# Kernel tuning notes

Measured on AMD Instinct MI355X. Metric: run time of the kernel, lower is better.

## Reference

```python
import jax, jax.numpy as jnp
import numpy as np


def _ln(x, w, b):
    m = x.mean(-1, keepdims=True)
    v = ((x - m) ** 2).mean(-1, keepdims=True)
    return (x - m) / jnp.sqrt(v + 1e-5) * w + b


def setup_inputs() -> dict:
    key = jax.random.key(0)
    ks = jax.random.split(key, 8)
    N, C, H, W = 2, 64, 128, 128
    heads, ksz = 2, 7
    C4 = 4 * C
    p = lambda k, shape: jax.random.normal(k, shape, dtype=jnp.float32) * 0.02
    return {
        "x": jax.random.normal(ks[0], (N, C, H, W), dtype=jnp.float32),
        "qkv_w": p(ks[1], (3 * C, C)),
        "qkv_b": jnp.zeros((3 * C,), jnp.float32),
        "proj_w": p(ks[2], (C, C)),
        "proj_b": jnp.zeros((C,), jnp.float32),
        "rpb": p(ks[3], (heads, 2 * ksz - 1, 2 * ksz - 1)),
        "ln1_w": jnp.ones((C,), jnp.float32),
        "ln1_b": jnp.zeros((C,), jnp.float32),
        "ln2_w": jnp.ones((C,), jnp.float32),
        "ln2_b": jnp.zeros((C,), jnp.float32),
        "fc1_w": p(ks[4], (C4, C)),
        "fc1_b": jnp.zeros((C4,), jnp.float32),
        "fc2_w": p(ks[5], (C, C4)),
        "fc2_b": jnp.zeros((C,), jnp.float32),
    }


def reference(x, qkv_w, qkv_b, proj_w, proj_b, rpb, ln1_w, ln1_b, ln2_w, ln2_b,
              fc1_w, fc1_b, fc2_w, fc2_b):
    N, C, H, W = x.shape
    heads = rpb.shape[0]
    ksz = (rpb.shape[1] + 1) // 2  # kernel size from (2k-1) bias table
    dh = C // heads

    xt = x.transpose(0, 2, 3, 1).reshape(N, H * W, C)  # n (h w) c
    shortcut = xt
    xn = _ln(xt, ln1_w, ln1_b).reshape(N, H, W, C)

    # qkv projection -> (3, N, heads, H, W, dh)
    qkv = (xn @ qkv_w.T + qkv_b).reshape(N, H, W, 3, heads, dh)
    qkv = qkv.transpose(3, 0, 4, 1, 2, 5)
    q = qkv[0] * (dh ** -0.5)
    k = qkv[1]
    v = qkv[2]

    # NATTEN neighborhood: window start clamped so every query sees k x k keys
    sh = jnp.clip(jnp.arange(H) - ksz // 2, 0, H - ksz)
    sw = jnp.clip(jnp.arange(W) - ksz // 2, 0, W - ksz)
    rows = sh[:, None] + jnp.arange(ksz)  # (H, k) key row indices
    cols = sw[:, None] + jnp.arange(ksz)  # (W, k) key col indices

    # relative position bias index: (query - key) + (k-1) in [0, 2k-2]
    rel_h = jnp.arange(H)[:, None] - rows + (ksz - 1)  # (H, k)
    rel_w = jnp.arange(W)[:, None] - cols + (ksz - 1)  # (W, k)
    bias = rpb[:, rel_h][:, :, :, rel_w]               # (heads, H, k, W, k)
    bias = bias.transpose(0, 1, 3, 2, 4)               # (heads, H, W, k, k)

    ri = rows[:, None, :, None]  # (H,1,k,1)
    ci = cols[None, :, None, :]  # (1,W,1,k)
    kwin = k[:, :, ri, ci, :]    # (N, heads, H, W, k, k, dh)
    vwin = v[:, :, ri, ci, :]

    scores = jnp.einsum('nzhwd,nzhwijd->nzhwij', q, kwin) + bias[None]
    attn = jax.nn.softmax(scores.reshape(N, heads, H, W, ksz * ksz), axis=-1)
    out = jnp.einsum('nzhwe,nzhwed->nzhwd', attn,
                     vwin.reshape(N, heads, H, W, ksz * ksz, dh))
    out = out.transpose(0, 2, 3, 1, 4).reshape(N, H, W, C) @ proj_w.T + proj_b

    x2 = shortcut + out.reshape(N, H * W, C)
    y = _ln(x2, ln2_w, ln2_b)
    y = jax.nn.gelu(y @ fc1_w.T + fc1_b, approximate=False) @ fc2_w.T + fc2_b
    x3 = x2 + y
    return x3.reshape(N, H, W, C).transpose(0, 3, 1, 2)
```

## Files before the change

kernel.cpp:

```cpp
#include <hip/hip_runtime.h>
#include <math.h>

#define TQ   32768
#define HWSZ 16384
#define CC   64
#define HH   128
#define WW   128
#define C3   192
#define C4   256
#define KS   7

typedef _Float16 half2v __attribute__((ext_vector_type(2)));
typedef _Float16 half4v __attribute__((ext_vector_type(4)));
typedef _Float16 half8v __attribute__((ext_vector_type(8)));
typedef float    f32x4  __attribute__((ext_vector_type(4)));

#define MFMA16(a, b, c) __builtin_amdgcn_mfma_f32_16x16x32_f16((a), (b), (c), 0, 0, 0)

__global__ __launch_bounds__(256) void k_qkvln(const float* __restrict__ x,
        const float* __restrict__ lnw, const float* __restrict__ lnb,
        const float* __restrict__ qw, const float* __restrict__ qb,
        const float* __restrict__ pw, const float* __restrict__ f1w,
        const float* __restrict__ f2w,
        _Float16* __restrict__ qkv16, _Float16* __restrict__ pw16,
        _Float16* __restrict__ f1w16, _Float16* __restrict__ f2w16) {
    __shared__ union {
        struct { __align__(16) _Float16 A[128 * 72]; __align__(16) _Float16 B[192 * 72]; } st;
        __align__(16) _Float16 outb[128 * 200];
    } u;
    __shared__ float ps1[256], ps2[256], m_s[128], r_s[128];
    __shared__ float w_s[64], b_s[64], bias_s[192];
    int tid = threadIdx.x;
    int t0 = blockIdx.x * 128;
    if (tid < 64) { w_s[tid] = lnw[tid]; b_s[tid] = lnb[tid]; }
    if (tid < 192) bias_s[tid] = qb[tid];
    int tok = tid & 127, cq = tid >> 7;
    int t = t0 + tok;
    int n = t >> 14, hw = t & (HWSZ - 1);
    const float* xr = x + ((size_t)n << 20) + hw;
    float v[32];
    float s = 0.f, s2 = 0.f;
#pragma unroll
    for (int e = 0; e < 32; ++e) {
        float f = xr[(cq * 32 + e) * HWSZ];
        v[e] = f; s += f; s2 += f * f;
    }
    ps1[tid] = s; ps2[tid] = s2;
    for (int i = tid; i < 3072; i += 256) {
        int jj = i >> 4, seg = i & 15;
        float4 v4 = *(const float4*)&qw[(size_t)jj * 64 + seg * 4];
        half4v h4 = { (_Float16)v4.x, (_Float16)v4.y, (_Float16)v4.z, (_Float16)v4.w };
        *(half4v*)&u.st.B[jj * 72 + seg * 4] = h4;
    }
    {
        int g = blockIdx.x * 256 + tid;
        if (g < 4096) pw16[g] = (_Float16)pw[g];
        else if (g < 20480) f1w16[g - 4096] = (_Float16)f1w[g - 4096];
        else if (g < 36864) f2w16[g - 20480] = (_Float16)f2w[g - 20480];
    }
    __syncthreads();
    if (tid < 128) {
        float ss = ps1[tid] + ps1[tid + 128];
        float qq = ps2[tid] + ps2[tid + 128];
        float m = ss * (1.f / 64.f);
        float var = qq * (1.f / 64.f) - m * m;
        m_s[tid] = m; r_s[tid] = rsqrtf(var + 1e-5f);
    }
    __syncthreads();
    {
        float m = m_s[tok], r = r_s[tok];
#pragma unroll
        for (int u8 = 0; u8 < 4; ++u8) {
            half8v o;
#pragma unroll
            for (int e = 0; e < 8; ++e) {
                int c = cq * 32 + u8 * 8 + e;
                o[e] = (_Float16)((v[u8 * 8 + e] - m) * r * w_s[c] + b_s[c]);
            }
            *(half8v*)&u.st.A[tok * 72 + cq * 32 + u8 * 8] = o;
        }
    }
    __syncthreads();
    int lane = tid & 63, wv = tid >> 6;
    int quad = lane >> 4, l16 = lane & 15;
    int mt0 = (wv & 1) * 64, nt0 = (wv >> 1) * 96;
    f32x4 acc[4][6];
#pragma unroll
    for (int mf = 0; mf < 4; ++mf)
#pragma unroll
        for (int nf = 0; nf < 6; ++nf) acc[mf][nf] = (f32x4){0.f, 0.f, 0.f, 0.f};
#pragma unroll
    for (int ks = 0; ks < 64; ks += 32) {
        half8v a[4], bfr[6];
#pragma unroll
        for (int mf = 0; mf < 4; ++mf)
            a[mf] = *(const half8v*)&u.st.A[(mt0 + mf * 16 + l16) * 72 + ks + quad * 8];
#pragma unroll
        for (int nf = 0; nf < 6; ++nf)
            bfr[nf] = *(const half8v*)&u.st.B[(nt0 + nf * 16 + l16) * 72 + ks + quad * 8];
#pragma unroll
        for (int mf = 0; mf < 4; ++mf)
#pragma unroll
            for (int nf = 0; nf < 6; ++nf) acc[mf][nf] = MFMA16(a[mf], bfr[nf], acc[mf][nf]);
    }
    __syncthreads();
    const float qscale = 0.17677669529663687f;
#pragma unroll
    for (int mf = 0; mf < 4; ++mf)
#pragma unroll
        for (int nf = 0; nf < 6; ++nf) {
            int j = nt0 + nf * 16 + l16;
            float bias = bias_s[j];
            float sc = (j < 64) ? qscale : 1.f;
#pragma unroll
            for (int r = 0; r < 4; ++r) {
                int tl = mt0 + mf * 16 + quad * 4 + r;
                u.outb[tl * 200 + j] = (_Float16)((acc[mf][nf][r] + bias) * sc);
            }
        }
    __syncthreads();
    for (int i = tid; i < 4096; i += 256) {
        int tk = i >> 5, rem = i & 31;
        if (rem < 24)
            *(half8v*)&qkv16[(size_t)(t0 + tk) * C3 + rem * 8] =
                *(const half8v*)&u.outb[tk * 200 + rem * 8];
    }
}

__global__ __launch_bounds__(256) void k_attnproj(const _Float16* __restrict__ qkv16,
        const float* __restrict__ rpb,
        const _Float16* __restrict__ pw16, const float* __restrict__ pb,
        const float* __restrict__ x,
        const float* __restrict__ ln2w, const float* __restrict__ ln2b,
        _Float16* __restrict__ x2_16, _Float16* __restrict__ xn2_16) {
    __shared__ __align__(16) char smem[77704];
    _Float16* kv_s  = (_Float16*)smem;
    _Float16* q_s   = (_Float16*)(smem + 53312);
    _Float16* s_s   = (_Float16*)(smem + 63552);
    float*    rpb_s = (float*)(smem + 76352);
    float* x2t  = (float*)smem;
    float* ps1  = (float*)(smem + 20480);
    float* ps2  = (float*)(smem + 21504);
    float* m_s  = (float*)(smem + 22528);
    float* r_s  = (float*)(smem + 22784);
    float* w_s  = (float*)(smem + 23040);
    float* b_s  = (float*)(smem + 23296);
    float* pb_s = (float*)(smem + 23552);

    int tid = threadIdx.x;
    int bx = blockIdx.x;
    int n  = bx >> 8;
    int th = (bx >> 4) & 15, tw = bx & 15;
    int h0 = th * 8, w0 = tw * 8;
    int wr0 = min(max(h0 - 3, 0), HH - 14);
    int ww0 = min(max(w0 - 3, 0), WW - 14);
    int tbase = n << 14;
    int lane = tid & 63, wvi = tid >> 6;
    int quad = lane >> 4, l16 = lane & 15;

    for (int i = tid; i < 338; i += 256) rpb_s[i] = rpb[i];
    for (int i = tid; i < 196 * 16; i += 256) {
        int tok = i >> 4, u = i & 15;
        int wi = tok / 14, wj = tok - wi * 14;
        *(half8v*)&kv_s[tok * 136 + u * 8] = *(const half8v*)&qkv16[
            (size_t)(tbase + (wr0 + wi) * WW + ww0 + wj) * C3 + 64 + u * 8];
    }
    for (int i = tid; i < 64 * 8; i += 256) {
        int q = i >> 3, u = i & 7;
        int qg = tbase + (h0 + (q >> 3)) * WW + (w0 + (q & 7));
        *(half8v*)&q_s[q * 80 + u * 8] = *(const half8v*)&qkv16[(size_t)qg * C3 + u * 8];
    }
    __syncthreads();

    int c16 = tid & 1, z = (tid >> 1) & 1, q = tid >> 2;
    int qy = q >> 3, qx = q & 7;
    int h = h0 + qy, wc = w0 + qx;
    int sh = min(max(h - 3, 0), HH - KS);
    int sw = min(max(wc - 3, 0), WW - KS);
    int oh = sh - wr0, ow = sw - ww0;
    int dhp = h - sh + 6, dwp = wc - sw + 6;
    {
        const half8v* qp = (const half8v*)&q_s[q * 80 + z * 32];
        half8v q0 = qp[0], q1 = qp[1], q2 = qp[2], q3 = qp[3];
        int i7 = 0, j7 = c16;
        for (int nb = c16; nb < 49; nb += 2) {
            int tok = (oh + i7) * 14 + (ow + j7);
            const half8v* kp = (const half8v*)&kv_s[tok * 136 + z * 32];
            half2v acc2 = { (_Float16)0.f, (_Float16)0.f };
            half8v k0 = kp[0], k1 = kp[1], k2 = kp[2], k3 = kp[3];
            acc2 += (half2v){k0.s0, k0.s1} * (half2v){q0.s0, q0.s1};
            acc2 += (half2v){k0.s2, k0.s3} * (half2v){q0.s2, q0.s3};
            acc2 += (half2v){k0.s4, k0.s5} * (half2v){q0.s4, q0.s5};
            acc2 += (half2v){k0.s6, k0.s7} * (half2v){q0.s6, q0.s7};
            acc2 += (half2v){k1.s0, k1.s1} * (half2v){q1.s0, q1.s1};
            acc2 += (half2v){k1.s2, k1.s3} * (half2v){q1.s2, q1.s3};
            acc2 += (half2v){k1.s4, k1.s5} * (half2v){q1.s4, q1.s5};
            acc2 += (half2v){k1.s6, k1.s7} * (half2v){q1.s6, q1.s7};
            acc2 += (half2v){k2.s0, k2.s1} * (half2v){q2.s0, q2.s1};
            acc2 += (half2v){k2.s2, k2.s3} * (half2v){q2.s2, q2.s3};
            acc2 += (half2v){k2.s4, k2.s5} * (half2v){q2.s4, q2.s5};
            acc2 += (half2v){k2.s6, k2.s7} * (half2v){q2.s6, q2.s7};
            acc2 += (half2v){k3.s0, k3.s1} * (half2v){q3.s0, q3.s1};
            acc2 += (half2v){k3.s2, k3.s3} * (half2v){q3.s2, q3.s3};
            acc2 += (half2v){k3.s4, k3.s5} * (half2v){q3.s4, q3.s5};
            acc2 += (half2v){k3.s6, k3.s7} * (half2v){q3.s6, q3.s7};
            float s = (float)acc2.x + (float)acc2.y
                    + rpb_s[(z * 13 + (dhp - i7)) * 13 + (dwp - j7)];
            s_s[(q * 2 + z) * 50 + nb] = (_Float16)s;
            j7 += 2;
            if (j7 >= 7) { j7 -= 7; ++i7; }
        }
    }
    __syncthreads();

    if (tid < 128) {
        _Float16* sp = &s_s[tid * 50];
        float mx = -1e30f;
        for (int i = 0; i < 49; ++i) mx = fmaxf(mx, (float)sp[i]);
        float sum = 0.f;
        for (int i = 0; i < 49; ++i) {
            float e = __expf((float)sp[i] - mx);
            sum += e;
            sp[i] = (_Float16)e;
        }
        float inv = 1.f / sum;
        for (int i = 0; i < 49; ++i) sp[i] = (_Float16)((float)sp[i] * inv);
    }
    __syncthreads();

    {
        const _Float16* pp = &s_s[(q * 2 + z) * 50];
        half2v acc[8];
#pragma unroll
        for (int j = 0; j < 8; ++j) acc[j] = (half2v){ (_Float16)0.f, (_Float16)0.f };
        int i7 = 0, j7 = 0;
        for (int nb = 0; nb < 49; ++nb) {
            int tok = (oh + i7) * 14 + (ow + j7);
            _Float16 p = pp[nb];
            half2v p2 = { p, p };
            const half8v* vp = (const half8v*)&kv_s[tok * 136 + 64 + z * 32 + c16 * 16];
            half8v v0 = vp[0], v1 = vp[1];
            acc[0] += (half2v){v0.s0, v0.s1} * p2;
            acc[1] += (half2v){v0.s2, v0.s3} * p2;
            acc[2] += (half2v){v0.s4, v0.s5} * p2;
            acc[3] += (half2v){v0.s6, v0.s7} * p2;
            acc[4] += (half2v){v1.s0, v1.s1} * p2;
            acc[5] += (half2v){v1.s2, v1.s3} * p2;
            acc[6] += (half2v){v1.s4, v1.s5} * p2;
            acc[7] += (half2v){v1.s6, v1.s7} * p2;
            ++j7;
            if (j7 == 7) { j7 = 0; ++i7; }
        }
        _Float16* op = q_s + q * 72 + z * 32 + c16 * 16;
        half8v o0 = {acc[0].x, acc[0].y, acc[1].x, acc[1].y, acc[2].x, acc[2].y, acc[3].x, acc[3].y};
        half8v o1 = {acc[4].x, acc[4].y, acc[5].x, acc[5].y, acc[6].x, acc[6].y, acc[7].x, acc[7].y};
        *(half8v*)op = o0;
        *(half8v*)(op + 8) = o1;
    }
    __syncthreads();
    for (int i = tid; i < 512; i += 256) {
        int jj = i >> 3, c8 = i & 7;
        *(half8v*)&s_s[jj * 72 + c8 * 8] = *(const half8v*)&pw16[jj * 64 + c8 * 8];
    }
    if (tid < 64) { w_s[tid] = ln2w[tid]; b_s[tid] = ln2b[tid]; pb_s[tid] = pb[tid]; }
    __syncthreads();
    {
        int mt0 = wvi * 16;
        f32x4 acc2[4];
#pragma unroll
        for (int nf = 0; nf < 4; ++nf) acc2[nf] = (f32x4){0.f, 0.f, 0.f, 0.f};
#pragma unroll
        for (int ks = 0; ks < 64; ks += 32) {
            half8v a = *(const half8v*)&q_s[(mt0 + l16) * 72 + ks + quad * 8];
            half8v bfr[4];
#pragma unroll
            for (int nf = 0; nf < 4; ++nf)
                bfr[nf] = *(const half8v*)&s_s[(nf * 16 + l16) * 72 + ks + quad * 8];
#pragma unroll
            for (int nf = 0; nf < 4; ++nf) acc2[nf] = MFMA16(a, bfr[nf], acc2[nf]);
        }
        __syncthreads();
        int tl0 = mt0 + quad * 4;
        int hwl = (h0 + (tl0 >> 3)) * WW + w0 + (tl0 & 7);
#pragma unroll
        for (int nf = 0; nf < 4; ++nf) {
            int j = nf * 16 + l16;
            float bias = pb_s[j];
            float4 rx = *(const float4*)&x[((size_t)(n * CC + j) << 14) + hwl];
#pragma unroll
            for (int r = 0; r < 4; ++r)
                x2t[(tl0 + r) * 68 + j] = acc2[nf][r] + bias + ((const float*)&rx)[r];
        }
    }
    __syncthreads();
    int tok = tid & 63, cq = tid >> 6;
    {
        float s = 0.f, s2 = 0.f;
#pragma unroll
        for (int e = 0; e < 16; ++e) {
            float f = x2t[tok * 68 + cq * 16 + e];
            s += f; s2 += f * f;
        }
        ps1[tid] = s; ps2[tid] = s2;
    }
    __syncthreads();
    if (tid < 64) {
        float ss = ps1[tid] + ps1[64 + tid] + ps1[128 + tid] + ps1[192 + tid];
        float qq = ps2[tid] + ps2[64 + tid] + ps2[128 + tid] + ps2[192 + tid];
        float m = ss * (1.f / 64.f);
        float var = qq * (1.f / 64.f) - m * m;
        m_s[tid] = m; r_s[tid] = rsqrtf(var + 1e-5f);
    }
    __syncthreads();
    {
        float m = m_s[tok], r = r_s[tok];
        int qg = tbase + (h0 + (tok >> 3)) * WW + (w0 + (tok & 7));
        half8v hv0, hv1, nv0, nv1;
#pragma unroll
        for (int e = 0; e < 8; ++e) {
            int c = cq * 16 + e;
            float f = x2t[tok * 68 + c];
            hv0[e] = (_Float16)f;
            nv0[e] = (_Float16)((f - m) * r * w_s[c] + b_s[c]);
        }
#pragma unroll
        for (int e = 0; e < 8; ++e) {
            int c = cq * 16 + 8 + e;
            float f = x2t[tok * 68 + c];
            hv1[e] = (_Float16)f;
            nv1[e] = (_Float16)((f - m) * r * w_s[c] + b_s[c]);
        }
        size_t base = (size_t)qg * 64 + cq * 16;
        *(half8v*)&x2_16[base] = hv0;  *(half8v*)&x2_16[base + 8] = hv1;
        *(half8v*)&xn2_16[base] = nv0; *(half8v*)&xn2_16[base + 8] = nv1;
    }
}

__global__ __launch_bounds__(256) void k_mlp(const _Float16* __restrict__ xn2,
        const _Float16* __restrict__ x2_16,
        const _Float16* __restrict__ f1w16, const float* __restrict__ f1b,
        const _Float16* __restrict__ f2w16, const float* __restrict__ f2b,
        float* __restrict__ out) {
    __shared__ __align__(16) _Float16 H_s[64 * 264];
    __shared__ union {
        struct { __align__(16) _Float16 A[64 * 72]; __align__(16) _Float16 B[128 * 72]; } st;
        float tr[64 * 68];
    } u;
    __shared__ float f1b_s[256], f2b_s[64];
    int tid = threadIdx.x;
    int t0 = blockIdx.x * 64;
    int lane = tid & 63, wv = tid >> 6;
    int quad = lane >> 4, l16 = lane & 15;
    f1b_s[tid] = f1b[tid];
    if (tid < 64) f2b_s[tid] = f2b[tid];
    for (int i = tid; i < 512; i += 256) {
        int tok = i >> 3, u8 = i & 7;
        *(half8v*)&u.st.A[tok * 72 + u8 * 8] = *(const half8v*)&xn2[(size_t)(t0 + tok) * 64 + u8 * 8];
    }
    for (int jh = 0; jh < 2; ++jh) {
        if (jh) __syncthreads();
        for (int i = tid; i < 1024; i += 256) {
            int jj = i >> 3, c8 = i & 7;
            *(half8v*)&u.st.B[jj * 72 + c8 * 8] =
                *(const half8v*)&f1w16[(size_t)(jh * 128 + jj) * 64 + c8 * 8];
        }
        __syncthreads();
        int mt0 = (wv & 1) * 32, nt0 = (wv >> 1) * 64;
        f32x4 acc[2][4];
#pragma unroll
        for (int mf = 0; mf < 2; ++mf)
#pragma unroll
            for (int nf = 0; nf < 4; ++nf) acc[mf][nf] = (f32x4){0.f, 0.f, 0.f, 0.f};
#pragma unroll
        for (int ks = 0; ks < 64; ks += 32) {
            half8v a[2], bfr[4];
#pragma unroll
            for (int mf = 0; mf < 2; ++mf)
                a[mf] = *(const half8v*)&u.st.A[(mt0 + mf * 16 + l16) * 72 + ks + quad * 8];
#pragma unroll
            for (int nf = 0; nf < 4; ++nf)
                bfr[nf] = *(const half8v*)&u.st.B[(nt0 + nf * 16 + l16) * 72 + ks + quad * 8];
#pragma unroll
            for (int mf = 0; mf < 2; ++mf)
#pragma unroll
                for (int nf = 0; nf < 4; ++nf) acc[mf][nf] = MFMA16(a[mf], bfr[nf], acc[mf][nf]);
        }
#pragma unroll
        for (int mf = 0; mf < 2; ++mf)
#pragma unroll
            for (int nf = 0; nf < 4; ++nf) {
                int jl = nt0 + nf * 16 + l16;
                float bias = f1b_s[jh * 128 + jl];
#pragma unroll
                for (int r = 0; r < 4; ++r) {
                    int tl = mt0 + mf * 16 + quad * 4 + r;
                    float vv = acc[mf][nf][r] + bias;
                    float g = 0.5f * vv * (1.f + erff(vv * 0.70710678118654752f));
                    H_s[tl * 264 + jh * 128 + jl] = (_Float16)g;
                }
            }
    }
    __syncthreads();
    int mt0 = wv * 16;
    f32x4 acc2[4];
#pragma unroll
    for (int nf = 0; nf < 4; ++nf) acc2[nf] = (f32x4){0.f, 0.f, 0.f, 0.f};
    for (int kp = 0; kp < 4; ++kp) {
        if (kp) __syncthreads();
        for (int i = tid; i < 512; i += 256) {
            int jj = i >> 3, c8 = i & 7;
            *(half8v*)&u.st.B[jj * 72 + c8 * 8] =
                *(const half8v*)&f2w16[(size_t)jj * C4 + kp * 64 + c8 * 8];
        }
        __syncthreads();
#pragma unroll
        for (int ks = 0; ks < 64; ks += 32) {
            half8v a = *(const half8v*)&H_s[(mt0 + l16) * 264 + kp * 64 + ks + quad * 8];
            half8v bfr[4];
#pragma unroll
            for (int nf = 0; nf < 4; ++nf)
                bfr[nf] = *(const half8v*)&u.st.B[(nf * 16 + l16) * 72 + ks + quad * 8];
#pragma unroll
            for (int nf = 0; nf < 4; ++nf) acc2[nf] = MFMA16(a, bfr[nf], acc2[nf]);
        }
    }
    __syncthreads();
#pragma unroll
    for (int nf = 0; nf < 4; ++nf) {
        int j = nf * 16 + l16;
        float bias = f2b_s[j];
#pragma unroll
        for (int r = 0; r < 4; ++r) {
            int tl = mt0 + quad * 4 + r;
            float v = acc2[nf][r] + bias + (float)x2_16[(size_t)(t0 + tl) * 64 + j];
            u.tr[j * 68 + tl] = v;
        }
    }
    __syncthreads();
    int n = t0 >> 14, hw0 = t0 & (HWSZ - 1);
    for (int i = tid; i < 1024; i += 256) {
        int j = i >> 4, seg = i & 15;
        float4 v = *(const float4*)&u.tr[j * 68 + seg * 4];
        *(float4*)&out[((size_t)(n * CC + j) << 14) + hw0 + seg * 4] = v;
    }
}

extern "C" void kernel_launch(void* const* d_in, const int* in_sizes, int n_in,
                              void* d_out, int out_size, void* d_ws, size_t ws_size,
                              hipStream_t stream) {
    const float* x      = (const float*)d_in[0];
    const float* qkv_w  = (const float*)d_in[1];
    const float* qkv_b  = (const float*)d_in[2];
    const float* proj_w = (const float*)d_in[3];
    const float* proj_b = (const float*)d_in[4];
    const float* rpb    = (const float*)d_in[5];
    const float* ln1_w  = (const float*)d_in[6];
    const float* ln1_b  = (const float*)d_in[7];
    const float* ln2_w  = (const float*)d_in[8];
    const float* ln2_b  = (const float*)d_in[9];
    const float* fc1_w  = (const float*)d_in[10];
    const float* fc1_b  = (const float*)d_in[11];
    const float* fc2_w  = (const float*)d_in[12];
    const float* fc2_b  = (const float*)d_in[13];
    float* out = (float*)d_out;
    char* ws = (char*)d_ws;

    _Float16* qkv16  = (_Float16*)(ws);
    _Float16* x2_16  = (_Float16*)(ws + 12582912);
    _Float16* xn2_16 = (_Float16*)(ws + 16777216);
    _Float16* pw16   = (_Float16*)(ws + 20971520);
    _Float16* f1w16  = (_Float16*)(ws + 20979712);
    _Float16* f2w16  = (_Float16*)(ws + 21012480);

    k_qkvln   <<<256, 256, 0, stream>>>(x, ln1_w, ln1_b, qkv_w, qkv_b,
                                        proj_w, fc1_w, fc2_w,
                                        qkv16, pw16, f1w16, f2w16);
    k_attnproj<<<512, 256, 0, stream>>>(qkv16, rpb, pw16, proj_b, x, ln2_w, ln2_b,
                                        x2_16, xn2_16);
    k_mlp     <<<512, 256, 0, stream>>>(xn2_16, x2_16, f1w16, fc1_b, f2w16, fc2_b, out);
}
```

Baseline: 132.6 us.

## Keep full MLP weights resident in LDS and process two token tiles per block

```diff
diff --git a/kernel.cpp b/kernel.cpp
--- a/kernel.cpp
+++ b/kernel.cpp
@@ -336,112 +336,116 @@
     }
 }
 
-__global__ __launch_bounds__(256) void k_mlp(const _Float16* __restrict__ xn2,
+__global__ __launch_bounds__(512, 1) void k_mlp(const _Float16* __restrict__ xn2,
         const _Float16* __restrict__ x2_16,
         const _Float16* __restrict__ f1w16, const float* __restrict__ f1b,
         const _Float16* __restrict__ f2w16, const float* __restrict__ f2b,
         float* __restrict__ out) {
-    __shared__ __align__(16) _Float16 H_s[64 * 264];
+    __shared__ __align__(16) _Float16 W1[256 * 72];
+    __shared__ __align__(16) _Float16 W2[64 * 264];
+    __shared__ __align__(16) _Float16 A_s[64 * 72];
     __shared__ union {
-        struct { __align__(16) _Float16 A[64 * 72]; __align__(16) _Float16 B[128 * 72]; } st;
+        __align__(16) _Float16 H[64 * 264];
         float tr[64 * 68];
     } u;
     __shared__ float f1b_s[256], f2b_s[64];
     int tid = threadIdx.x;
-    int t0 = blockIdx.x * 64;
     int lane = tid & 63, wv = tid >> 6;
     int quad = lane >> 4, l16 = lane & 15;
-    f1b_s[tid] = f1b[tid];
-    if (tid < 64) f2b_s[tid] = f2b[tid];
-    for (int i = tid; i < 512; i += 256) {
-        int tok = i >> 3, u8 = i & 7;
-        *(half8v*)&u.st.A[tok * 72 + u8 * 8] = *(const half8v*)&xn2[(size_t)(t0 + tok) * 64 + u8 * 8];
-    }
-    for (int jh = 0; jh < 2; ++jh) {
-        if (jh) __syncthreads();
-        for (int i = tid; i < 1024; i += 256) {
-            int jj = i >> 3, c8 = i & 7;
-            *(half8v*)&u.st.B[jj * 72 + c8 * 8] =
-                *(const half8v*)&f1w16[(size_t)(jh * 128 + jj) * 64 + c8 * 8];
+    for (int i = tid; i < 2048; i += 512) {
+        int jj = i >> 3, c8 = i & 7;
+        *(half8v*)&W1[jj * 72 + c8 * 8] = *(const half8v*)&f1w16[(size_t)jj * 64 + c8 * 8];
+    }
+    for (int i = tid; i < 2048; i += 512) {
+        int jj = i >> 5, c8 = i & 31;
+        *(half8v*)&W2[jj * 264 + c8 * 8] = *(const half8v*)&f2w16[(size_t)jj * 256 + c8 * 8];
+    }
+    if (tid < 256) f1b_s[tid] = f1b[tid];
+    else if (tid < 320) f2b_s[tid - 256] = f2b[tid - 256];
+
+    for (int tt = 0; tt < 2; ++tt) {
+        int t0 = blockIdx.x * 128 + tt * 64;
+        {
+            int tok = tid >> 3, u8 = tid & 7;
+            *(half8v*)&A_s[tok * 72 + u8 * 8] =
+                *(const half8v*)&xn2[(size_t)(t0 + tok) * 64 + u8 * 8];
         }
         __syncthreads();
-        int mt0 = (wv & 1) * 32, nt0 = (wv >> 1) * 64;
-        f32x4 acc[2][4];
-#pragma unroll
-        for (int mf = 0; mf < 2; ++mf)
-#pragma unroll
-            for (int nf = 0; nf < 4; ++nf) acc[mf][nf] = (f32x4){0.f, 0.f, 0.f, 0.f};
-#pragma unroll
-        for (int ks = 0; ks < 64; ks += 32) {
-            half8v a[2], bfr[4];
+        {
+            int mt0 = (wv & 1) * 32, nt0 = (wv >> 1) * 64;
+            f32x4 acc[2][4];
 #pragma unroll
             for (int mf = 0; mf < 2; ++mf)
-                a[mf] = *(const half8v*)&u.st.A[(mt0 + mf * 16 + l16) * 72 + ks + quad * 8];
-#pragma unroll
-            for (int nf = 0; nf < 4; ++nf)
-                bfr[nf] = *(const half8v*)&u.st.B[(nt0 + nf * 16 + l16) * 72 + ks + quad * 8];
+#pragma unroll
+                for (int nf = 0; nf < 4; ++nf) acc[mf][nf] = (f32x4){0.f, 0.f, 0.f, 0.f};
+#pragma unroll
+            for (int ks = 0; ks < 64; ks += 32) {
+                half8v a[2], bfr[4];
+#pragma unroll
+                for (int mf = 0; mf < 2; ++mf)
+                    a[mf] = *(const half8v*)&A_s[(mt0 + mf * 16 + l16) * 72 + ks + quad * 8];
+#pragma unroll
+                for (int nf = 0; nf < 4; ++nf)
+                    bfr[nf] = *(const half8v*)&W1[(nt0 + nf * 16 + l16) * 72 + ks + quad * 8];
+#pragma unroll
+                for (int mf = 0; mf < 2; ++mf)
+#pragma unroll
+                    for (int nf = 0; nf < 4; ++nf) acc[mf][nf] = MFMA16(a[mf], bfr[nf], acc[mf][nf]);
+            }
 #pragma unroll
             for (int mf = 0; mf < 2; ++mf)
 #pragma unroll
-                for (int nf = 0; nf < 4; ++nf) acc[mf][nf] = MFMA16(a[mf], bfr[nf], acc[mf][nf]);
-        }
-#pragma unroll
-        for (int mf = 0; mf < 2; ++mf)
-#pragma unroll
-            for (int nf = 0; nf < 4; ++nf) {
-                int jl = nt0 + nf * 16 + l16;
-                float bias = f1b_s[jh * 128 + jl];
+                for (int nf = 0; nf < 4; ++nf) {
+                    int jl = nt0 + nf * 16 + l16;
+                    float bias = f1b_s[jl];
+#pragma unroll
+                    for (int r = 0; r < 4; ++r) {
+                        int tl = mt0 + mf * 16 + quad * 4 + r;
+                        float vv = acc[mf][nf][r] + bias;
+                        float g = 0.5f * vv * (1.f + erff(vv * 0.70710678118654752f));
+                        u.H[tl * 264 + jl] = (_Float16)g;
+                    }
+                }
+        }
+        __syncthreads();
+        {
+            int mt = (wv & 3) * 16, n0 = (wv >> 2) * 32;
+            f32x4 acc2[2];
+#pragma unroll
+            for (int nf = 0; nf < 2; ++nf) acc2[nf] = (f32x4){0.f, 0.f, 0.f, 0.f};
+#pragma unroll
+            for (int ks = 0; ks < 256; ks += 32) {
+                half8v a = *(const half8v*)&u.H[(mt + l16) * 264 + ks + quad * 8];
+                half8v bfr[2];
+#pragma unroll
+                for (int nf = 0; nf < 2; ++nf)
+                    bfr[nf] = *(const half8v*)&W2[(n0 + nf * 16 + l16) * 264 + ks + quad * 8];
+#pragma unroll
+                for (int nf = 0; nf < 2; ++nf) acc2[nf] = MFMA16(a, bfr[nf], acc2[nf]);
+            }
+            __syncthreads();
+#pragma unroll
+            for (int nf = 0; nf < 2; ++nf) {
+                int j = n0 + nf * 16 + l16;
+                float bias = f2b_s[j];
 #pragma unroll
                 for (int r = 0; r < 4; ++r) {
-                    int tl = mt0 + mf * 16 + quad * 4 + r;
-                    float vv = acc[mf][nf][r] + bias;
-                    float g = 0.5f * vv * (1.f + erff(vv * 0.70710678118654752f));
-                    H_s[tl * 264 + jh * 128 + jl] = (_Float16)g;
+                    int tl = mt + quad * 4 + r;
+                    float v = acc2[nf][r] + bias + (float)x2_16[(size_t)(t0 + tl) * 64 + j];
+                    u.tr[j * 68 + tl] = v;
                 }
             }
-    }
-    __syncthreads();
-    int mt0 = wv * 16;
-    f32x4 acc2[4];
-#pragma unroll
-    for (int nf = 0; nf < 4; ++nf) acc2[nf] = (f32x4){0.f, 0.f, 0.f, 0.f};
-    for (int kp = 0; kp < 4; ++kp) {
-        if (kp) __syncthreads();
-        for (int i = tid; i < 512; i += 256) {
-            int jj = i >> 3, c8 = i & 7;
-            *(half8v*)&u.st.B[jj * 72 + c8 * 8] =
-                *(const half8v*)&f2w16[(size_t)jj * C4 + kp * 64 + c8 * 8];
         }
         __syncthreads();
-#pragma unroll
-        for (int ks = 0; ks < 64; ks += 32) {
-            half8v a = *(const half8v*)&H_s[(mt0 + l16) * 264 + kp * 64 + ks + quad * 8];
-            half8v bfr[4];
-#pragma unroll
-            for (int nf = 0; nf < 4; ++nf)
-                bfr[nf] = *(const half8v*)&u.st.B[(nf * 16 + l16) * 72 + ks + quad * 8];
-#pragma unroll
-            for (int nf = 0; nf < 4; ++nf) acc2[nf] = MFMA16(a, bfr[nf], acc2[nf]);
-        }
-    }
-    __syncthreads();
-#pragma unroll
-    for (int nf = 0; nf < 4; ++nf) {
-        int j = nf * 16 + l16;
-        float bias = f2b_s[j];
-#pragma unroll
-        for (int r = 0; r < 4; ++r) {
-            int tl = mt0 + quad * 4 + r;
-            float v = acc2[nf][r] + bias + (float)x2_16[(size_t)(t0 + tl) * 64 + j];
-            u.tr[j * 68 + tl] = v;
-        }
-    }
-    __syncthreads();
-    int n = t0 >> 14, hw0 = t0 & (HWSZ - 1);
-    for (int i = tid; i < 1024; i += 256) {
-        int j = i >> 4, seg = i & 15;
-        float4 v = *(const float4*)&u.tr[j * 68 + seg * 4];
-        *(float4*)&out[((size_t)(n * CC + j) << 14) + hw0 + seg * 4] = v;
+        {
+            int n = t0 >> 14, hw0 = t0 & (HWSZ - 1);
+            for (int i = tid; i < 1024; i += 512) {
+                int j = i >> 4, seg = i & 15;
+                float4 v = *(const float4*)&u.tr[j * 68 + seg * 4];
+                *(float4*)&out[((size_t)(n * CC + j) << 14) + hw0 + seg * 4] = v;
+            }
+        }
+        __syncthreads();
     }
 }
 
@@ -477,5 +481,5 @@
                                         qkv16, pw16, f1w16, f2w16);
     k_attnproj<<<512, 256, 0, stream>>>(qkv16, rpb, pw16, proj_b, x, ln2_w, ln2_b,
                                         x2_16, xn2_16);
-    k_mlp     <<<512, 256, 0, stream>>>(xn2_16, x2_16, f1w16, fc1_b, f2w16, fc2_b, out);
+    k_mlp     <<<256, 512, 0, stream>>>(xn2_16, x2_16, f1w16, fc1_b, f2w16, fc2_b, out);
 }
```

New measurement: 128.5 us. 1.03x faster.

## Halve qkv tile to 64 tokens and restructure MLP kernel weight staging

Applied to the files above, without the earlier changes.

```diff
diff --git a/kernel.cpp b/kernel.cpp
--- a/kernel.cpp
+++ b/kernel.cpp
@@ -25,24 +25,24 @@
         _Float16* __restrict__ qkv16, _Float16* __restrict__ pw16,
         _Float16* __restrict__ f1w16, _Float16* __restrict__ f2w16) {
     __shared__ union {
-        struct { __align__(16) _Float16 A[128 * 72]; __align__(16) _Float16 B[192 * 72]; } st;
-        __align__(16) _Float16 outb[128 * 200];
+        struct { __align__(16) _Float16 A[64 * 72]; __align__(16) _Float16 B[192 * 72]; } st;
+        __align__(16) _Float16 outb[64 * 200];
     } u;
-    __shared__ float ps1[256], ps2[256], m_s[128], r_s[128];
+    __shared__ float ps1[256], ps2[256], m_s[64], r_s[64];
     __shared__ float w_s[64], b_s[64], bias_s[192];
     int tid = threadIdx.x;
-    int t0 = blockIdx.x * 128;
+    int t0 = blockIdx.x * 64;
     if (tid < 64) { w_s[tid] = lnw[tid]; b_s[tid] = lnb[tid]; }
     if (tid < 192) bias_s[tid] = qb[tid];
-    int tok = tid & 127, cq = tid >> 7;
+    int tok = tid & 63, cq = tid >> 6;
     int t = t0 + tok;
     int n = t >> 14, hw = t & (HWSZ - 1);
     const float* xr = x + ((size_t)n << 20) + hw;
-    float v[32];
+    float v[16];
     float s = 0.f, s2 = 0.f;
 #pragma unroll
-    for (int e = 0; e < 32; ++e) {
-        float f = xr[(cq * 32 + e) * HWSZ];
+    for (int e = 0; e < 16; ++e) {
+        float f = xr[(cq * 16 + e) * HWSZ];
         v[e] = f; s += f; s2 += f * f;
     }
     ps1[tid] = s; ps2[tid] = s2;
@@ -59,9 +59,9 @@
         else if (g < 36864) f2w16[g - 20480] = (_Float16)f2w[g - 20480];
     }
     __syncthreads();
-    if (tid < 128) {
-        float ss = ps1[tid] + ps1[tid + 128];
-        float qq = ps2[tid] + ps2[tid + 128];
+    if (tid < 64) {
+        float ss = ps1[tid] + ps1[64 + tid] + ps1[128 + tid] + ps1[192 + tid];
+        float qq = ps2[tid] + ps2[64 + tid] + ps2[128 + tid] + ps2[192 + tid];
         float m = ss * (1.f / 64.f);
         float var = qq * (1.f / 64.f) - m * m;
         m_s[tid] = m; r_s[tid] = rsqrtf(var + 1e-5f);
@@ -69,44 +69,47 @@
     __syncthreads();
     {
         float m = m_s[tok], r = r_s[tok];
-#pragma unroll
-        for (int u8 = 0; u8 < 4; ++u8) {
-            half8v o;
-#pragma unroll
-            for (int e = 0; e < 8; ++e) {
-                int c = cq * 32 + u8 * 8 + e;
-                o[e] = (_Float16)((v[u8 * 8 + e] - m) * r * w_s[c] + b_s[c]);
-            }
-            *(half8v*)&u.st.A[tok * 72 + cq * 32 + u8 * 8] = o;
-        }
+        half8v o0, o1;
+#pragma unroll
+        for (int e = 0; e < 8; ++e) {
+            int c = cq * 16 + e;
+            o0[e] = (_Float16)((v[e] - m) * r * w_s[c] + b_s[c]);
+        }
+#pragma unroll
+        for (int e = 0; e < 8; ++e) {
+            int c = cq * 16 + 8 + e;
+            o1[e] = (_Float16)((v[8 + e] - m) * r * w_s[c] + b_s[c]);
+        }
+        *(half8v*)&u.st.A[tok * 72 + cq * 16] = o0;
+        *(half8v*)&u.st.A[tok * 72 + cq * 16 + 8] = o1;
     }
     __syncthreads();
     int lane = tid & 63, wv = tid >> 6;
     int quad = lane >> 4, l16 = lane & 15;
-    int mt0 = (wv & 1) * 64, nt0 = (wv >> 1) * 96;
-    f32x4 acc[4][6];
-#pragma unroll
-    for (int mf = 0; mf < 4; ++mf)
+    int mt0 = (wv & 1) * 32, nt0 = (wv >> 1) * 96;
+    f32x4 acc[2][6];
+#pragma unroll
+    for (int mf = 0; mf < 2; ++mf)
 #pragma unroll
         for (int nf = 0; nf < 6; ++nf) acc[mf][nf] = (f32x4){0.f, 0.f, 0.f, 0.f};
 #pragma unroll
     for (int ks = 0; ks < 64; ks += 32) {
-        half8v a[4], bfr[6];
-#pragma unroll
-        for (int mf = 0; mf < 4; ++mf)
+        half8v a[2], bfr[6];
+#pragma unroll
+        for (int mf = 0; mf < 2; ++mf)
             a[mf] = *(const half8v*)&u.st.A[(mt0 + mf * 16 + l16) * 72 + ks + quad * 8];
 #pragma unroll
         for (int nf = 0; nf < 6; ++nf)
             bfr[nf] = *(const half8v*)&u.st.B[(nt0 + nf * 16 + l16) * 72 + ks + quad * 8];
 #pragma unroll
-        for (int mf = 0; mf < 4; ++mf)
+        for (int mf = 0; mf < 2; ++mf)
 #pragma unroll
             for (int nf = 0; nf < 6; ++nf) acc[mf][nf] = MFMA16(a[mf], bfr[nf], acc[mf][nf]);
     }
     __syncthreads();
     const float qscale = 0.17677669529663687f;
 #pragma unroll
-    for (int mf = 0; mf < 4; ++mf)
+    for (int mf = 0; mf < 2; ++mf)
 #pragma unroll
         for (int nf = 0; nf < 6; ++nf) {
             int j = nt0 + nf * 16 + l16;
@@ -119,7 +122,7 @@
             }
         }
     __syncthreads();
-    for (int i = tid; i < 4096; i += 256) {
+    for (int i = tid; i < 2048; i += 256) {
         int tk = i >> 5, rem = i & 31;
         if (rem < 24)
             *(half8v*)&qkv16[(size_t)(t0 + tk) * C3 + rem * 8] =
@@ -341,9 +344,9 @@
         const _Float16* __restrict__ f1w16, const float* __restrict__ f1b,
         const _Float16* __restrict__ f2w16, const float* __restrict__ f2b,
         float* __restrict__ out) {
-    __shared__ __align__(16) _Float16 H_s[64 * 264];
+    __shared__ __align__(16) _Float16 W1[256 * 72];
     __shared__ union {
-        struct { __align__(16) _Float16 A[64 * 72]; __align__(16) _Float16 B[128 * 72]; } st;
+        __align__(16) _Float16 H[64 * 264];
         float tr[64 * 68];
     } u;
     __shared__ float f1b_s[256], f2b_s[64];
@@ -351,78 +354,62 @@
     int t0 = blockIdx.x * 64;
     int lane = tid & 63, wv = tid >> 6;
     int quad = lane >> 4, l16 = lane & 15;
+    for (int i = tid; i < 2048; i += 256) {
+        int jj = i >> 3, c8 = i & 7;
+        *(half8v*)&W1[jj * 72 + c8 * 8] = *(const half8v*)&f1w16[(size_t)jj * 64 + c8 * 8];
+    }
     f1b_s[tid] = f1b[tid];
     if (tid < 64) f2b_s[tid] = f2b[tid];
-    for (int i = tid; i < 512; i += 256) {
-        int tok = i >> 3, u8 = i & 7;
-        *(half8v*)&u.st.A[tok * 72 + u8 * 8] = *(const half8v*)&xn2[(size_t)(t0 + tok) * 64 + u8 * 8];
-    }
-    for (int jh = 0; jh < 2; ++jh) {
-        if (jh) __syncthreads();
-        for (int i = tid; i < 1024; i += 256) {
-            int jj = i >> 3, c8 = i & 7;
-            *(half8v*)&u.st.B[jj * 72 + c8 * 8] =
-                *(const half8v*)&f1w16[(size_t)(jh * 128 + jj) * 64 + c8 * 8];
-        }
-        __syncthreads();
-        int mt0 = (wv & 1) * 32, nt0 = (wv >> 1) * 64;
-        f32x4 acc[2][4];
+    __syncthreads();
+    {
+        int mt0 = (wv & 1) * 32, nt0 = (wv >> 1) * 128;
+        f32x4 acc[2][8];
 #pragma unroll
         for (int mf = 0; mf < 2; ++mf)
 #pragma unroll
-            for (int nf = 0; nf < 4; ++nf) acc[mf][nf] = (f32x4){0.f, 0.f, 0.f, 0.f};
+            for (int nf = 0; nf < 8; ++nf) acc[mf][nf] = (f32x4){0.f, 0.f, 0.f, 0.f};
 #pragma unroll
         for (int ks = 0; ks < 64; ks += 32) {
-            half8v a[2], bfr[4];
+            half8v a[2];
 #pragma unroll
             for (int mf = 0; mf < 2; ++mf)
-                a[mf] = *(const half8v*)&u.st.A[(mt0 + mf * 16 + l16) * 72 + ks + quad * 8];
-#pragma unroll
-            for (int nf = 0; nf < 4; ++nf)
-                bfr[nf] = *(const half8v*)&u.st.B[(nt0 + nf * 16 + l16) * 72 + ks + quad * 8];
-#pragma unroll
-            for (int mf = 0; mf < 2; ++mf)
-#pragma unroll
-                for (int nf = 0; nf < 4; ++nf) acc[mf][nf] = MFMA16(a[mf], bfr[nf], acc[mf][nf]);
+                a[mf] = *(const half8v*)&xn2[(size_t)(t0 + mt0 + mf * 16 + l16) * 64 + ks + quad * 8];
+#pragma unroll
+            for (int nf = 0; nf < 8; ++nf) {
+                half8v bfr = *(const half8v*)&W1[(nt0 + nf * 16 + l16) * 72 + ks + quad * 8];
+#pragma unroll
+                for (int mf = 0; mf < 2; ++mf) acc[mf][nf] = MFMA16(a[mf], bfr, acc[mf][nf]);
+            }
         }
 #pragma unroll
         for (int mf = 0; mf < 2; ++mf)
 #pragma unroll
-            for (int nf = 0; nf < 4; ++nf) {
+            for (int nf = 0; nf < 8; ++nf) {
                 int jl = nt0 + nf * 16 + l16;
-                float bias = f1b_s[jh * 128 + jl];
+                float bias = f1b_s[jl];
 #pragma unroll
                 for (int r = 0; r < 4; ++r) {
                     int tl = mt0 + mf * 16 + quad * 4 + r;
                     float vv = acc[mf][nf][r] + bias;
                     float g = 0.5f * vv * (1.f + erff(vv * 0.70710678118654752f));
-                    H_s[tl * 264 + jh * 128 + jl] = (_Float16)g;
+                    u.H[tl * 264 + jl] = (_Float16)g;
                 }
             }
     }
     __syncthreads();
-    int mt0 = wv * 16;
+    int mt = wv * 16;
     f32x4 acc2[4];
 #pragma unroll
     for (int nf = 0; nf < 4; ++nf) acc2[nf] = (f32x4){0.f, 0.f, 0.f, 0.f};
-    for (int kp = 0; kp < 4; ++kp) {
-        if (kp) __syncthreads();
-        for (int i = tid; i < 512; i += 256) {
-            int jj = i >> 3, c8 = i & 7;
-            *(half8v*)&u.st.B[jj * 72 + c8 * 8] =
-                *(const half8v*)&f2w16[(size_t)jj * C4 + kp * 64 + c8 * 8];
-        }
-        __syncthreads();
-#pragma unroll
-        for (int ks = 0; ks < 64; ks += 32) {
-            half8v a = *(const half8v*)&H_s[(mt0 + l16) * 264 + kp * 64 + ks + quad * 8];
-            half8v bfr[4];
-#pragma unroll
-            for (int nf = 0; nf < 4; ++nf)
-                bfr[nf] = *(const half8v*)&u.st.B[(nf * 16 + l16) * 72 + ks + quad * 8];
-#pragma unroll
-            for (int nf = 0; nf < 4; ++nf) acc2[nf] = MFMA16(a, bfr[nf], acc2[nf]);
-        }
+#pragma unroll
+    for (int ks = 0; ks < 256; ks += 32) {
+        half8v a = *(const half8v*)&u.H[(mt + l16) * 264 + ks + quad * 8];
+        half8v bfr[4];
+#pragma unroll
+        for (int nf = 0; nf < 4; ++nf)
+            bfr[nf] = *(const half8v*)&f2w16[(size_t)(nf * 16 + l16) * 256 + ks + quad * 8];
+#pragma unroll
+        for (int nf = 0; nf < 4; ++nf) acc2[nf] = MFMA16(a, bfr[nf], acc2[nf]);
     }
     __syncthreads();
 #pragma unroll
@@ -431,7 +418,7 @@
         float bias = f2b_s[j];
 #pragma unroll
         for (int r = 0; r < 4; ++r) {
-            int tl = mt0 + quad * 4 + r;
+            int tl = mt + quad * 4 + r;
             float v = acc2[nf][r] + bias + (float)x2_16[(size_t)(t0 + tl) * 64 + j];
             u.tr[j * 68 + tl] = v;
         }
@@ -472,7 +459,7 @@
     _Float16* f1w16  = (_Float16*)(ws + 20979712);
     _Float16* f2w16  = (_Float16*)(ws + 21012480);
 
-    k_qkvln   <<<256, 256, 0, stream>>>(x, ln1_w, ln1_b, qkv_w, qkv_b,
+    k_qkvln   <<<512, 256, 0, stream>>>(x, ln1_w, ln1_b, qkv_w, qkv_b,
                                         proj_w, fc1_w, fc2_w,
                                         qkv16, pw16, f1w16, f2w16);
     k_attnproj<<<512, 256, 0, stream>>>(qkv16, rpb, pw16, proj_b, x, ln2_w, ln2_b,
```

After: 132.7 us. No clear change (+0.1%).

## Load MLP operands directly from global memory instead of staging in LDS

Applied to the files above, without the earlier changes.

```diff
diff --git a/kernel.cpp b/kernel.cpp
--- a/kernel.cpp
+++ b/kernel.cpp
@@ -341,9 +341,8 @@
         const _Float16* __restrict__ f1w16, const float* __restrict__ f1b,
         const _Float16* __restrict__ f2w16, const float* __restrict__ f2b,
         float* __restrict__ out) {
-    __shared__ __align__(16) _Float16 H_s[64 * 264];
     __shared__ union {
-        struct { __align__(16) _Float16 A[64 * 72]; __align__(16) _Float16 B[128 * 72]; } st;
+        __align__(16) _Float16 H[64 * 264];
         float tr[64 * 68];
     } u;
     __shared__ float f1b_s[256], f2b_s[64];
@@ -353,76 +352,56 @@
     int quad = lane >> 4, l16 = lane & 15;
     f1b_s[tid] = f1b[tid];
     if (tid < 64) f2b_s[tid] = f2b[tid];
-    for (int i = tid; i < 512; i += 256) {
-        int tok = i >> 3, u8 = i & 7;
-        *(half8v*)&u.st.A[tok * 72 + u8 * 8] = *(const half8v*)&xn2[(size_t)(t0 + tok) * 64 + u8 * 8];
-    }
-    for (int jh = 0; jh < 2; ++jh) {
-        if (jh) __syncthreads();
-        for (int i = tid; i < 1024; i += 256) {
-            int jj = i >> 3, c8 = i & 7;
-            *(half8v*)&u.st.B[jj * 72 + c8 * 8] =
-                *(const half8v*)&f1w16[(size_t)(jh * 128 + jj) * 64 + c8 * 8];
-        }
-        __syncthreads();
-        int mt0 = (wv & 1) * 32, nt0 = (wv >> 1) * 64;
-        f32x4 acc[2][4];
+    __syncthreads();
+    {
+        int mt0 = (wv & 1) * 32, nt0 = (wv >> 1) * 128;
+        f32x4 acc[2][8];
 #pragma unroll
         for (int mf = 0; mf < 2; ++mf)
 #pragma unroll
-            for (int nf = 0; nf < 4; ++nf) acc[mf][nf] = (f32x4){0.f, 0.f, 0.f, 0.f};
+            for (int nf = 0; nf < 8; ++nf) acc[mf][nf] = (f32x4){0.f, 0.f, 0.f, 0.f};
 #pragma unroll
         for (int ks = 0; ks < 64; ks += 32) {
-            half8v a[2], bfr[4];
+            half8v a[2];
 #pragma unroll
             for (int mf = 0; mf < 2; ++mf)
-                a[mf] = *(const half8v*)&u.st.A[(mt0 + mf * 16 + l16) * 72 + ks + quad * 8];
-#pragma unroll
-            for (int nf = 0; nf < 4; ++nf)
-                bfr[nf] = *(const half8v*)&u.st.B[(nt0 + nf * 16 + l16) * 72 + ks + quad * 8];
-#pragma unroll
-            for (int mf = 0; mf < 2; ++mf)
-#pragma unroll
-                for (int nf = 0; nf < 4; ++nf) acc[mf][nf] = MFMA16(a[mf], bfr[nf], acc[mf][nf]);
+                a[mf] = *(const half8v*)&xn2[(size_t)(t0 + mt0 + mf * 16 + l16) * 64 + ks + quad * 8];
+#pragma unroll
+            for (int nf = 0; nf < 8; ++nf) {
+                half8v bfr = *(const half8v*)&f1w16[(size_t)(nt0 + nf * 16 + l16) * 64 + ks + quad * 8];
+#pragma unroll
+                for (int mf = 0; mf < 2; ++mf) acc[mf][nf] = MFMA16(a[mf], bfr, acc[mf][nf]);
+            }
         }
 #pragma unroll
         for (int mf = 0; mf < 2; ++mf)
 #pragma unroll
-            for (int nf = 0; nf < 4; ++nf) {
+            for (int nf = 0; nf < 8; ++nf) {
                 int jl = nt0 + nf * 16 + l16;
-                float bias = f1b_s[jh * 128 + jl];
+                float bias = f1b_s[jl];
 #pragma unroll
                 for (int r = 0; r < 4; ++r) {
                     int tl = mt0 + mf * 16 + quad * 4 + r;
                     float vv = acc[mf][nf][r] + bias;
                     float g = 0.5f * vv * (1.f + erff(vv * 0.70710678118654752f));
-                    H_s[tl * 264 + jh * 128 + jl] = (_Float16)g;
+                    u.H[tl * 264 + jl] = (_Float16)g;
                 }
             }
     }
     __syncthreads();
-    int mt0 = wv * 16;
+    int mt = wv * 16;
     f32x4 acc2[4];
 #pragma unroll
     for (int nf = 0; nf < 4; ++nf) acc2[nf] = (f32x4){0.f, 0.f, 0.f, 0.f};
-    for (int kp = 0; kp < 4; ++kp) {
-        if (kp) __syncthreads();
-        for (int i = tid; i < 512; i += 256) {
-            int jj = i >> 3, c8 = i & 7;
-            *(half8v*)&u.st.B[jj * 72 + c8 * 8] =
-                *(const half8v*)&f2w16[(size_t)jj * C4 + kp * 64 + c8 * 8];
-        }
-        __syncthreads();
-#pragma unroll
-        for (int ks = 0; ks < 64; ks += 32) {
-            half8v a = *(const half8v*)&H_s[(mt0 + l16) * 264 + kp * 64 + ks + quad * 8];
-            half8v bfr[4];
-#pragma unroll
-            for (int nf = 0; nf < 4; ++nf)
-                bfr[nf] = *(const half8v*)&u.st.B[(nf * 16 + l16) * 72 + ks + quad * 8];
-#pragma unroll
-            for (int nf = 0; nf < 4; ++nf) acc2[nf] = MFMA16(a, bfr[nf], acc2[nf]);
-        }
+#pragma unroll
+    for (int ks = 0; ks < 256; ks += 32) {
+        half8v a = *(const half8v*)&u.H[(mt + l16) * 264 + ks + quad * 8];
+        half8v bfr[4];
+#pragma unroll
+        for (int nf = 0; nf < 4; ++nf)
+            bfr[nf] = *(const half8v*)&f2w16[(size_t)(nf * 16 + l16) * 256 + ks + quad * 8];
+#pragma unroll
+        for (int nf = 0; nf < 4; ++nf) acc2[nf] = MFMA16(a, bfr[nf], acc2[nf]);
     }
     __syncthreads();
 #pragma unroll
@@ -431,7 +410,7 @@
         float bias = f2b_s[j];
 #pragma unroll
         for (int r = 0; r < 4; ++r) {
-            int tl = mt0 + quad * 4 + r;
+            int tl = mt + quad * 4 + r;
             float v = acc2[nf][r] + bias + (float)x2_16[(size_t)(t0 + tl) * 64 + j];
             u.tr[j * 68 + tl] = v;
         }
```

Measured after the change: 136.0 us. +2.6%, slower.
